# Optimization experiments

Hardware: AMD Instinct MI355X
Metric: run time of the kernel (lower is better)

Reference implementation:

```python
import jax, jax.numpy as jnp
import numpy as np

CUTOFF = 5.0
B, A, N, G, F = 32, 256, 64, 50, 128


def _ssp(v):
    # shifted softplus used by SchNet filter network
    return jax.nn.softplus(v) - jnp.log(2.0).astype(v.dtype)


def setup_inputs() -> dict:
    key = jax.random.key(0)
    ks = jax.random.split(key, 8)
    x = jax.random.normal(ks[0], (B, A, F), dtype=jnp.float32)
    r_ij = jax.random.uniform(ks[1], (B, A, N), dtype=jnp.float32) * 4.5
    f_ij = jax.random.normal(ks[2], (B, A, N, G), dtype=jnp.float32)
    pairwise_mask = jnp.ones((B, A, N), dtype=jnp.float32)
    neighbors = jax.random.randint(ks[3], (B, A, N), 0, A, dtype=jnp.int64)
    in2f_w = jax.random.normal(ks[4], (F, F), dtype=jnp.float32) / np.sqrt(F)
    fw1 = jax.random.normal(ks[5], (G, F), dtype=jnp.float32) / np.sqrt(G)
    fb1 = jnp.zeros((F,), dtype=jnp.float32)
    fw2 = jax.random.normal(ks[6], (F, F), dtype=jnp.float32) / np.sqrt(F)
    fb2 = jnp.zeros((F,), dtype=jnp.float32)
    return {"x": x, "r_ij": r_ij, "f_ij": f_ij, "pairwise_mask": pairwise_mask,
            "neighbors": neighbors, "in2f_w": in2f_w, "fw1": fw1, "fb1": fb1,
            "fw2": fw2, "fb2": fb2}


def reference(x, r_ij, f_ij, pairwise_mask, neighbors, in2f_w, fw1, fb1, fw2, fb2):
    # filter network: Dense(G->F, shifted softplus) -> Dense(F->F, linear)
    W = _ssp(jnp.einsum('bang,gf->banf', f_ij, fw1) + fb1)
    W = jnp.einsum('banh,hf->banf', W, fw2) + fb2          # (B,A,N,F)
    # cosine cutoff
    C = 0.5 * (jnp.cos(r_ij * (jnp.pi / CUTOFF)) + 1.0)
    C = C * (r_ij < CUTOFF).astype(r_ij.dtype)
    W = W * C[..., None]
    # in2f dense (no bias)
    y = jnp.einsum('bai,if->baf', x, in2f_w)               # (B,A,F)
    # gather neighbor features along atom axis
    b_idx = jnp.arange(B)[:, None, None]
    y_nbh = y[b_idx, neighbors]                             # (B,A,N,F)
    # elementwise filter multiply + masked sum over neighbor axis
    out = jnp.sum(y_nbh * W * pairwise_mask[..., None], axis=2)  # (B,A,F)
    return out
```

## Files before the change

kernel.cpp:

```cpp
#include <hip/hip_runtime.h>
#include <hip/hip_bf16.h>
#include <math.h>

#define Bdim 32
#define Adim 256
#define Ndim 64
#define Gdim 50
#define Fdim 128

typedef __attribute__((ext_vector_type(8)))  short short8;
typedef __attribute__((ext_vector_type(16))) float floatx16;

__device__ __forceinline__ unsigned short f2bf_u(float x) {
    __hip_bfloat16 h = __float2bfloat16(x);
    return __builtin_bit_cast(unsigned short, h);
}
__device__ __forceinline__ unsigned pk2bf(float a, float b) {
    return (unsigned)f2bf_u(a) | ((unsigned)f2bf_u(b) << 16);
}
__device__ __forceinline__ float bf2f(unsigned short v) {
    return __builtin_bit_cast(float, ((unsigned)v) << 16);
}
__device__ __forceinline__ float sspf(float v) {
    float t = __expf(-fabsf(v));
    return fmaxf(v, 0.0f) +
           fmaf(__log2f(1.0f + t), 0.69314718056f, -0.69314718056f);
}
__device__ __forceinline__ short8 mk8(unsigned a, unsigned b, unsigned c, unsigned d) {
    union { unsigned u[4]; short8 s; } t;
    t.u[0] = a; t.u[1] = b; t.u[2] = c; t.u[3] = d;
    return t.s;
}

__global__ __launch_bounds__(256) void in2f_mfma2(const float* __restrict__ x,
                                                  const float* __restrict__ w,
                                                  unsigned short* __restrict__ y,
                                                  const float* __restrict__ fw1,
                                                  const float* __restrict__ fb1,
                                                  unsigned short* __restrict__ fw1t) {
    const int tid = threadIdx.x;
    if (blockIdx.x == 64) {
        for (int idx = tid; idx < 128 * 64; idx += 256) {
            int f = idx >> 6, g = idx & 63;
            float v = (g < Gdim) ? fw1[g * 128 + f] : ((g == Gdim) ? fb1[f] : 0.0f);
            fw1t[idx] = f2bf_u(v);
        }
        return;
    }
    __shared__ short sWT[128 * 132];
    __shared__ short sX [128 * 132];

#pragma unroll 4
    for (int k = 0; k < 32; ++k) {
        int idx = tid + k * 256;
        float2 v = *(const float2*)(w + 2 * idx);
        int i = idx >> 6;
        int f = (2 * idx) & 127;
        sWT[f * 132 + i]       = (short)f2bf_u(v.x);
        sWT[(f + 1) * 132 + i] = (short)f2bf_u(v.y);
    }
    const float* xb = x + (size_t)blockIdx.x * (128 * 128);
#pragma unroll 4
    for (int k = 0; k < 32; ++k) {
        int idx = tid + k * 256;
        float2 v = *(const float2*)(xb + 2 * idx);
        int row = idx >> 6;
        int i = (2 * idx) & 127;
        *(unsigned*)&sX[row * 132 + i] = pk2bf(v.x, v.y);
    }
    __syncthreads();

    const int wv = tid >> 6, lane = tid & 63, lm = lane & 31, lh = lane >> 5;
    floatx16 acc[4];
#pragma unroll
    for (int jt = 0; jt < 4; ++jt)
#pragma unroll
        for (int e = 0; e < 16; ++e) acc[jt][e] = 0.0f;

#pragma unroll
    for (int ks = 0; ks < 8; ++ks) {
        int g0 = ks * 16 + lh * 8;
        const short* ap = &sX[(wv * 32 + lm) * 132 + g0];
        uint2 a0 = *(const uint2*)ap;
        uint2 a1 = *(const uint2*)(ap + 4);
        short8 a = mk8(a0.x, a0.y, a1.x, a1.y);
#pragma unroll
        for (int jt = 0; jt < 4; ++jt) {
            const short* bp = &sWT[(jt * 32 + lm) * 132 + g0];
            uint2 b0 = *(const uint2*)bp;
            uint2 b1 = *(const uint2*)(bp + 4);
            acc[jt] = __builtin_amdgcn_mfma_f32_32x32x16_bf16(
                a, mk8(b0.x, b0.y, b1.x, b1.y), acc[jt], 0, 0, 0);
        }
    }
    const int rbase = blockIdx.x * 128 + wv * 32;
#pragma unroll
    for (int jt = 0; jt < 4; ++jt)
#pragma unroll
        for (int r = 0; r < 16; ++r) {
            int row = rbase + (r & 3) + 8 * (r >> 2) + 4 * lh;
            y[(size_t)row * 128 + jt * 32 + lm] = f2bf_u(acc[jt][r]);
        }
}

#define SF2 132
#define NSP 4096
#define GRID2 2048

struct FijRegs { float2 p[13]; };

__device__ __forceinline__ FijRegs load_fij(const float* __restrict__ f_ij,
                                            int sp, int row, int lh) {
    FijRegs F;
    const float* base = f_ij + (size_t)sp * (2 * Ndim * Gdim) + row * Gdim;
#pragma unroll
    for (int ks = 0; ks < 3; ++ks) {
        int g0 = 16 * ks + 8 * lh;
#pragma unroll
        for (int j = 0; j < 4; ++j)
            F.p[ks * 4 + j] = *(const float2*)(base + g0 + 2 * j);
    }
    F.p[12] = *(const float2*)(base + 48);
    return F;
}

__device__ __forceinline__ void cf_body(
    int sp, int par, const FijRegs& F, int nsp, FijRegs& Fn,
    const float* __restrict__ f_ij, const float* __restrict__ r_ij,
    const float* __restrict__ mask, const int* __restrict__ nbr,
    const unsigned short* __restrict__ fw1t,
    const unsigned short* __restrict__ ybf, float* __restrict__ out,
    float4 fb2v, const short* sFw2,
    float (*sRed)[2][128], int wv, int lm, int lh, int row)
{
    short8 bfr[4];
#pragma unroll
    for (int ks = 0; ks < 3; ++ks)
        bfr[ks] = mk8(pk2bf(F.p[ks*4+0].x, F.p[ks*4+0].y),
                      pk2bf(F.p[ks*4+1].x, F.p[ks*4+1].y),
                      pk2bf(F.p[ks*4+2].x, F.p[ks*4+2].y),
                      pk2bf(F.p[ks*4+3].x, F.p[ks*4+3].y));
    {
        unsigned u0 = lh ? 0u : pk2bf(F.p[12].x, F.p[12].y);
        unsigned u1 = lh ? 0u : 0x00003F80u;
        bfr[3] = mk8(u0, u1, 0u, 0u);
    }
    if (nsp >= 0) Fn = load_fij(f_ij, nsp, row, lh);

    unsigned A2[8][4];
#pragma unroll
    for (int ft = 0; ft < 4; ++ft) {
        floatx16 a1;
#pragma unroll
        for (int e = 0; e < 16; ++e) a1[e] = 0.0f;
        const unsigned short* fwp = fw1t + ((ft * 32 + lm) * 64 + lh * 8);
#pragma unroll
        for (int ks = 0; ks < 4; ++ks) {
            short8 a = *(const short8*)(fwp + ks * 16);
            a1 = __builtin_amdgcn_mfma_f32_32x32x16_bf16(a, bfr[ks], a1, 0, 0, 0);
        }
        unsigned P[8], X[8];
#pragma unroll
        for (int q = 0; q < 8; ++q)
            P[q] = pk2bf(sspf(a1[2 * q]), sspf(a1[2 * q + 1]));
#pragma unroll
        for (int q = 0; q < 8; ++q) X[q] = (unsigned)__shfl_xor((int)P[q], 32);
        A2[2*ft][0]   = lh ? X[2] : P[0];  A2[2*ft][1]   = lh ? X[3] : P[1];
        A2[2*ft][2]   = lh ? P[2] : X[0];  A2[2*ft][3]   = lh ? P[3] : X[1];
        A2[2*ft+1][0] = lh ? X[6] : P[4];  A2[2*ft+1][1] = lh ? X[7] : P[5];
        A2[2*ft+1][2] = lh ? P[6] : X[4];  A2[2*ft+1][3] = lh ? P[7] : X[5];
    }

    floatx16 acc2[4];
#pragma unroll
    for (int jt = 0; jt < 4; ++jt)
#pragma unroll
        for (int e = 0; e < 16; ++e) acc2[jt][e] = 0.0f;
#pragma unroll
    for (int ks = 0; ks < 8; ++ks) {
        short8 a = mk8(A2[ks][0], A2[ks][1], A2[ks][2], A2[ks][3]);
#pragma unroll
        for (int jt = 0; jt < 4; ++jt) {
            const short* bp = &sFw2[(jt * 32 + lm) * SF2 + ks * 16 + lh * 8];
            uint2 b0 = *(const uint2*)bp;
            uint2 b1 = *(const uint2*)(bp + 4);
            acc2[jt] = __builtin_amdgcn_mfma_f32_32x32x16_bf16(
                a, mk8(b0.x, b0.y, b1.x, b1.y), acc2[jt], 0, 0, 0);
        }
    }

    const int site = sp * 2 + (wv >> 1);
    float cmv[16]; int nbv[16];
#pragma unroll
    for (int rq = 0; rq < 4; ++rq) {
        int off = site * Ndim + (wv & 1) * 32 + rq * 8 + lh * 4;
        float4 r4 = *(const float4*)(r_ij + off);
        float4 m4 = *(const float4*)(mask + off);
        int4   n4 = *(const int4*)(nbr + off);
        float rr[4] = { r4.x, r4.y, r4.z, r4.w };
        float mm[4] = { m4.x, m4.y, m4.z, m4.w };
        int   nn[4] = { n4.x, n4.y, n4.z, n4.w };
#pragma unroll
        for (int j = 0; j < 4; ++j) {
            float c = 0.5f * (__cosf(rr[j] * 0.62831853071796f) + 1.0f);
            c = (rr[j] < 5.0f) ? c : 0.0f;
            cmv[rq * 4 + j] = c * mm[j];
            nbv[rq * 4 + j] = nn[j];
        }
    }

    const int bofs = (site >> 8) * Adim;
    float part[4] = {0.f, 0.f, 0.f, 0.f};
#pragma unroll
    for (int r = 0; r < 16; ++r) {
        float cm = cmv[r];
        const unsigned short* yr = ybf + (size_t)(bofs + nbv[r]) * Fdim;
#pragma unroll
        for (int jt = 0; jt < 4; ++jt) {
            float fb2j = (jt == 0) ? fb2v.x : (jt == 1) ? fb2v.y
                       : (jt == 2) ? fb2v.z : fb2v.w;
            float t = (acc2[jt][r] + fb2j) * cm;
            part[jt] = fmaf(t, bf2f(yr[jt * 32 + lm]), part[jt]);
        }
    }
#pragma unroll
    for (int jt = 0; jt < 4; ++jt) part[jt] += __shfl_xor(part[jt], 32);

    const int s = wv >> 1;
    if (wv & 1) {
#pragma unroll
        for (int k = 0; k < 2; ++k)
            sRed[par][s][(2 * lh + k) * 32 + lm] = part[2 * lh + k];
    }
    __syncthreads();
    if (!(wv & 1)) {
#pragma unroll
        for (int k = 0; k < 2; ++k) {
            int jt = 2 * lh + k;
            int f = jt * 32 + lm;
            out[(size_t)site * Fdim + f] = part[jt] + sRed[par][s][f];
        }
    }
}

__global__ __launch_bounds__(256, 4) void cfconv_mfma5(
    const float* __restrict__ r_ij, const float* __restrict__ f_ij,
    const float* __restrict__ mask, const int* __restrict__ nbr,
    const unsigned short* __restrict__ fw1t, const float* __restrict__ fw2,
    const float* __restrict__ fb2,
    const unsigned short* __restrict__ ybf, float* __restrict__ out)
{
    __shared__ short sFw2[128 * SF2];
    __shared__ float sRed[2][2][128];

    const int tid = threadIdx.x, wv = tid >> 6, lane = tid & 63;
    const int lm = lane & 31, lh = lane >> 5;
    const int bid = blockIdx.x;
    const int row = wv * 32 + lm;

    FijRegs FA = load_fij(f_ij, bid, row, lh);

    for (int idx = tid; idx < 128 * 128; idx += 256) {
        int h = idx >> 7, f = idx & 127;
        sFw2[f * SF2 + h] = (short)f2bf_u(fw2[idx]);
    }
    float4 fb2v;
    fb2v.x = fb2[lm]; fb2v.y = fb2[32 + lm]; fb2v.z = fb2[64 + lm]; fb2v.w = fb2[96 + lm];
    __syncthreads();

    const int sp1 = bid + GRID2;
    FijRegs FB;
    cf_body(bid, 0, FA, sp1, FB, f_ij, r_ij, mask, nbr, fw1t, ybf, out,
            fb2v, sFw2, sRed, wv, lm, lh, row);
    cf_body(sp1, 1, FB, -1, FA, f_ij, r_ij, mask, nbr, fw1t, ybf, out,
            fb2v, sFw2, sRed, wv, lm, lh, row);
}

extern "C" void kernel_launch(void* const* d_in, const int* in_sizes, int n_in,
                              void* d_out, int out_size, void* d_ws, size_t ws_size,
                              hipStream_t stream) {
    const float* x      = (const float*)d_in[0];
    const float* r_ij   = (const float*)d_in[1];
    const float* f_ij   = (const float*)d_in[2];
    const float* mask   = (const float*)d_in[3];
    const int*   nbr    = (const int*)d_in[4];
    const float* in2f_w = (const float*)d_in[5];
    const float* fw1    = (const float*)d_in[6];
    const float* fb1    = (const float*)d_in[7];
    const float* fw2    = (const float*)d_in[8];
    const float* fb2    = (const float*)d_in[9];
    float* out = (float*)d_out;
    unsigned short* y    = (unsigned short*)d_ws;
    unsigned short* fw1t = (unsigned short*)((char*)d_ws + (size_t)(Bdim*Adim*Fdim)*2);

    in2f_mfma2<<<65, 256, 0, stream>>>(x, in2f_w, y, fw1, fb1, fw1t);
    cfconv_mfma5<<<GRID2, 256, 0, stream>>>(r_ij, f_ij, mask, nbr,
                                            fw1t, fw2, fb2, y, out);
}
```

Before: 268.1 us.

## Precast fw2 once in prep kernel and stage filter activations through per-wave LDS

```diff
diff --git a/kernel.cpp b/kernel.cpp
--- a/kernel.cpp
+++ b/kernel.cpp
@@ -22,9 +22,8 @@
     return __builtin_bit_cast(float, ((unsigned)v) << 16);
 }
 __device__ __forceinline__ float sspf(float v) {
-    float t = __expf(-fabsf(v));
-    return fmaxf(v, 0.0f) +
-           fmaf(__log2f(1.0f + t), 0.69314718056f, -0.69314718056f);
+    float t = __expf(v);
+    return fmaf(__log2f(1.0f + t), 0.69314718056f, -0.69314718056f);
 }
 __device__ __forceinline__ short8 mk8(unsigned a, unsigned b, unsigned c, unsigned d) {
     union { unsigned u[4]; short8 s; } t;
@@ -37,13 +36,22 @@
                                                   unsigned short* __restrict__ y,
                                                   const float* __restrict__ fw1,
                                                   const float* __restrict__ fb1,
-                                                  unsigned short* __restrict__ fw1t) {
+                                                  const float* __restrict__ fw2,
+                                                  unsigned short* __restrict__ fw1t,
+                                                  unsigned short* __restrict__ fw2t) {
     const int tid = threadIdx.x;
     if (blockIdx.x == 64) {
         for (int idx = tid; idx < 128 * 64; idx += 256) {
             int f = idx >> 6, g = idx & 63;
             float v = (g < Gdim) ? fw1[g * 128 + f] : ((g == Gdim) ? fb1[f] : 0.0f);
             fw1t[idx] = f2bf_u(v);
+        }
+        return;
+    }
+    if (blockIdx.x == 65) {
+        for (int idx = tid; idx < 128 * 128; idx += 256) {
+            int f = idx >> 7, h = idx & 127;
+            fw2t[idx] = f2bf_u(fw2[h * 128 + f]);
         }
         return;
     }
@@ -103,7 +111,7 @@
         }
 }
 
-#define SF2 132
+#define SW1 136
 #define NSP 4096
 #define GRID2 2048
 
@@ -124,30 +132,28 @@
     return F;
 }
 
-__device__ __forceinline__ void cf_body(
-    int sp, int par, const FijRegs& F, int nsp, FijRegs& Fn,
-    const float* __restrict__ f_ij, const float* __restrict__ r_ij,
-    const float* __restrict__ mask, const int* __restrict__ nbr,
-    const unsigned short* __restrict__ fw1t,
-    const unsigned short* __restrict__ ybf, float* __restrict__ out,
-    float4 fb2v, const short* sFw2,
-    float (*sRed)[2][128], int wv, int lm, int lh, int row)
-{
-    short8 bfr[4];
+__device__ __forceinline__ void cvt_fij(const FijRegs& F, int lh, short8 bfr[4]) {
 #pragma unroll
     for (int ks = 0; ks < 3; ++ks)
         bfr[ks] = mk8(pk2bf(F.p[ks*4+0].x, F.p[ks*4+0].y),
                       pk2bf(F.p[ks*4+1].x, F.p[ks*4+1].y),
                       pk2bf(F.p[ks*4+2].x, F.p[ks*4+2].y),
                       pk2bf(F.p[ks*4+3].x, F.p[ks*4+3].y));
-    {
-        unsigned u0 = lh ? 0u : pk2bf(F.p[12].x, F.p[12].y);
-        unsigned u1 = lh ? 0u : 0x00003F80u;
-        bfr[3] = mk8(u0, u1, 0u, 0u);
-    }
-    if (nsp >= 0) Fn = load_fij(f_ij, nsp, row, lh);
-
-    unsigned A2[8][4];
+    unsigned u0 = lh ? 0u : pk2bf(F.p[12].x, F.p[12].y);
+    unsigned u1 = lh ? 0u : 0x00003F80u;
+    bfr[3] = mk8(u0, u1, 0u, 0u);
+}
+
+__device__ __forceinline__ void cf_body(
+    int sp, int par, const short8 bfr[4], int nsp, short8 bfrN[4],
+    const float* __restrict__ f_ij, const float* __restrict__ r_ij,
+    const float* __restrict__ mask, const int* __restrict__ nbr,
+    const unsigned short* __restrict__ fw1t,
+    const unsigned short* __restrict__ fw2t,
+    const unsigned short* __restrict__ ybf, float* __restrict__ out,
+    float4 fb2v, short* sW1w, float (*sRed)[2][128],
+    int wv, int lm, int lh, int row)
+{
 #pragma unroll
     for (int ft = 0; ft < 4; ++ft) {
         floatx16 a1;
@@ -159,17 +165,16 @@
             short8 a = *(const short8*)(fwp + ks * 16);
             a1 = __builtin_amdgcn_mfma_f32_32x32x16_bf16(a, bfr[ks], a1, 0, 0, 0);
         }
-        unsigned P[8], X[8];
-#pragma unroll
-        for (int q = 0; q < 8; ++q)
-            P[q] = pk2bf(sspf(a1[2 * q]), sspf(a1[2 * q + 1]));
-#pragma unroll
-        for (int q = 0; q < 8; ++q) X[q] = (unsigned)__shfl_xor((int)P[q], 32);
-        A2[2*ft][0]   = lh ? X[2] : P[0];  A2[2*ft][1]   = lh ? X[3] : P[1];
-        A2[2*ft][2]   = lh ? P[2] : X[0];  A2[2*ft][3]   = lh ? P[3] : X[1];
-        A2[2*ft+1][0] = lh ? X[6] : P[4];  A2[2*ft+1][1] = lh ? X[7] : P[5];
-        A2[2*ft+1][2] = lh ? P[6] : X[4];  A2[2*ft+1][3] = lh ? P[7] : X[5];
-    }
+#pragma unroll
+        for (int q = 0; q < 8; ++q) {
+            unsigned P = pk2bf(sspf(a1[2 * q]), sspf(a1[2 * q + 1]));
+            int h0 = ft * 32 + 4 * lh + 8 * (q >> 1) + 2 * (q & 1);
+            *(unsigned*)&sW1w[lm * SW1 + h0] = P;
+        }
+    }
+
+    FijRegs Fl;
+    if (nsp >= 0) Fl = load_fij(f_ij, nsp, row, lh);
 
     floatx16 acc2[4];
 #pragma unroll
@@ -178,16 +183,15 @@
         for (int e = 0; e < 16; ++e) acc2[jt][e] = 0.0f;
 #pragma unroll
     for (int ks = 0; ks < 8; ++ks) {
-        short8 a = mk8(A2[ks][0], A2[ks][1], A2[ks][2], A2[ks][3]);
+        short8 a = *(const short8*)&sW1w[lm * SW1 + ks * 16 + lh * 8];
 #pragma unroll
         for (int jt = 0; jt < 4; ++jt) {
-            const short* bp = &sFw2[(jt * 32 + lm) * SF2 + ks * 16 + lh * 8];
-            uint2 b0 = *(const uint2*)bp;
-            uint2 b1 = *(const uint2*)(bp + 4);
-            acc2[jt] = __builtin_amdgcn_mfma_f32_32x32x16_bf16(
-                a, mk8(b0.x, b0.y, b1.x, b1.y), acc2[jt], 0, 0, 0);
-        }
-    }
+            short8 b = *(const short8*)(fw2t + (jt * 32 + lm) * 128 + ks * 16 + lh * 8);
+            acc2[jt] = __builtin_amdgcn_mfma_f32_32x32x16_bf16(a, b, acc2[jt], 0, 0, 0);
+        }
+    }
+
+    if (nsp >= 0) cvt_fij(Fl, lh, bfrN);
 
     const int site = sp * 2 + (wv >> 1);
     float cmv[16]; int nbv[16];
@@ -243,37 +247,36 @@
     }
 }
 
-__global__ __launch_bounds__(256, 4) void cfconv_mfma5(
+__global__ __launch_bounds__(256, 4) void cfconv_mfma6(
     const float* __restrict__ r_ij, const float* __restrict__ f_ij,
     const float* __restrict__ mask, const int* __restrict__ nbr,
-    const unsigned short* __restrict__ fw1t, const float* __restrict__ fw2,
+    const unsigned short* __restrict__ fw1t,
+    const unsigned short* __restrict__ fw2t,
     const float* __restrict__ fb2,
     const unsigned short* __restrict__ ybf, float* __restrict__ out)
 {
-    __shared__ short sFw2[128 * SF2];
+    __shared__ short sW1[4][32][SW1];
     __shared__ float sRed[2][2][128];
 
     const int tid = threadIdx.x, wv = tid >> 6, lane = tid & 63;
     const int lm = lane & 31, lh = lane >> 5;
     const int bid = blockIdx.x;
     const int row = wv * 32 + lm;
-
-    FijRegs FA = load_fij(f_ij, bid, row, lh);
-
-    for (int idx = tid; idx < 128 * 128; idx += 256) {
-        int h = idx >> 7, f = idx & 127;
-        sFw2[f * SF2 + h] = (short)f2bf_u(fw2[idx]);
-    }
+    short* sW1w = &sW1[wv][0][0];
+
     float4 fb2v;
     fb2v.x = fb2[lm]; fb2v.y = fb2[32 + lm]; fb2v.z = fb2[64 + lm]; fb2v.w = fb2[96 + lm];
-    __syncthreads();
-
-    const int sp1 = bid + GRID2;
-    FijRegs FB;
-    cf_body(bid, 0, FA, sp1, FB, f_ij, r_ij, mask, nbr, fw1t, ybf, out,
-            fb2v, sFw2, sRed, wv, lm, lh, row);
-    cf_body(sp1, 1, FB, -1, FA, f_ij, r_ij, mask, nbr, fw1t, ybf, out,
-            fb2v, sFw2, sRed, wv, lm, lh, row);
+
+    short8 bA[4], bB[4];
+    {
+        FijRegs F0 = load_fij(f_ij, bid, row, lh);
+        cvt_fij(F0, lh, bA);
+    }
+
+    cf_body(bid, 0, bA, bid + GRID2, bB, f_ij, r_ij, mask, nbr,
+            fw1t, fw2t, ybf, out, fb2v, sW1w, sRed, wv, lm, lh, row);
+    cf_body(bid + GRID2, 1, bB, -1, bA, f_ij, r_ij, mask, nbr,
+            fw1t, fw2t, ybf, out, fb2v, sW1w, sRed, wv, lm, lh, row);
 }
 
 extern "C" void kernel_launch(void* const* d_in, const int* in_sizes, int n_in,
@@ -292,8 +295,9 @@
     float* out = (float*)d_out;
     unsigned short* y    = (unsigned short*)d_ws;
     unsigned short* fw1t = (unsigned short*)((char*)d_ws + (size_t)(Bdim*Adim*Fdim)*2);
-
-    in2f_mfma2<<<65, 256, 0, stream>>>(x, in2f_w, y, fw1, fb1, fw1t);
-    cfconv_mfma5<<<GRID2, 256, 0, stream>>>(r_ij, f_ij, mask, nbr,
-                                            fw1t, fw2, fb2, y, out);
-}
+    unsigned short* fw2t = fw1t + 128 * 64;
+
+    in2f_mfma2<<<66, 256, 0, stream>>>(x, in2f_w, y, fw1, fb1, fw2, fw1t, fw2t);
+    cfconv_mfma6<<<GRID2, 256, 0, stream>>>(r_ij, f_ij, mask, nbr,
+                                            fw1t, fw2t, fb2, y, out);
+}
```

Result: slower. 308.6 us (+15.1%).
